# Optimization experiments

Measured on AMD Instinct MI355X. Metric: run time of the kernel, lower is better.

## Reference

```python
import jax, jax.numpy as jnp
import numpy as np

D_MODEL = 1024
N_HEADS = 16
D_HEAD = D_MODEL // N_HEADS
NEG_INF = -1000000000.0


def setup_inputs() -> dict:
    key = jax.random.key(0)
    ks = jax.random.split(key, 12)
    B, S1, S2 = 2, 2048, 2048
    query = jax.random.normal(ks[0], (B, S1, D_MODEL), dtype=jnp.float32)
    k_in = jax.random.normal(ks[1], (B, S2, D_MODEL), dtype=jnp.float32)
    v_in = jax.random.normal(ks[2], (B, S2, D_MODEL), dtype=jnp.float32)
    # causal mask: True = position is masked out (filled with -1e9)
    mask = jnp.broadcast_to(jnp.triu(jnp.ones((S1, S2), dtype=bool), k=1), (B, S1, S2))
    s = 1.0 / np.sqrt(D_MODEL)
    W_q = jax.random.uniform(ks[3], (D_MODEL, D_MODEL), jnp.float32, -s, s)
    b_q = jax.random.uniform(ks[4], (D_MODEL,), jnp.float32, -s, s)
    W_k = jax.random.uniform(ks[5], (D_MODEL, D_MODEL), jnp.float32, -s, s)
    b_k = jax.random.uniform(ks[6], (D_MODEL,), jnp.float32, -s, s)
    W_v = jax.random.uniform(ks[7], (D_MODEL, D_MODEL), jnp.float32, -s, s)
    b_v = jax.random.uniform(ks[8], (D_MODEL,), jnp.float32, -s, s)
    W_o = jax.random.uniform(ks[9], (D_MODEL, D_MODEL), jnp.float32, -s, s)
    b_o = jax.random.uniform(ks[10], (D_MODEL,), jnp.float32, -s, s)
    return {"query": query, "key": k_in, "value": v_in, "mask": mask,
            "W_q": W_q, "b_q": b_q, "W_k": W_k, "b_k": b_k,
            "W_v": W_v, "b_v": b_v, "W_o": W_o, "b_o": b_o}


def reference(query, key, value, mask, W_q, b_q, W_k, b_k, W_v, b_v, W_o, b_o):
    B, S1, _ = query.shape
    S2 = key.shape[1]
    scalar = 1.0 / np.sqrt(D_HEAD)
    # projections (torch Linear: x @ W.T + b)
    Q = (query @ W_q.T + b_q).reshape(B, S1, N_HEADS, D_HEAD).transpose(0, 2, 1, 3)
    K = (key @ W_k.T + b_k).reshape(B, S2, N_HEADS, D_HEAD).transpose(0, 2, 1, 3)
    V = (value @ W_v.T + b_v).reshape(B, S2, N_HEADS, D_HEAD).transpose(0, 2, 1, 3)
    # [B, H, S1, S2]
    scores = jnp.einsum('bhqd,bhkd->bhqk', Q, K) * scalar
    scores = jnp.where(mask[:, None, :, :], NEG_INF, scores)
    probs = jax.nn.softmax(scores, axis=-1)
    attn = jnp.einsum('bhqk,bhkd->bhqd', probs, V)
    concat = attn.transpose(0, 2, 1, 3).reshape(B, S1, D_MODEL)
    return concat @ W_o.T + b_o
```

## Files before the change

### kernel.cpp

```cpp
#include <hip/hip_runtime.h>
#include <hip/hip_bf16.h>
#include <stdint.h>

typedef __bf16 bf16;
typedef __bf16 bf16x8 __attribute__((ext_vector_type(8)));
typedef float f32x4 __attribute__((ext_vector_type(4)));
typedef float f32x16 __attribute__((ext_vector_type(16)));
typedef unsigned int u32;
typedef u32 u32x4 __attribute__((ext_vector_type(4)));

#define D_MODEL 1024
#define S_LEN 2048
#define NB 2
#define NH 16
#define DH 64

__device__ __forceinline__ void gload_lds16(const bf16* g, bf16* l) {
    auto gp = reinterpret_cast<const __attribute__((address_space(1))) unsigned int*>(
        reinterpret_cast<uintptr_t>(g));
    auto lp = reinterpret_cast<__attribute__((address_space(3))) unsigned int*>(
        reinterpret_cast<uintptr_t>(l));
    __builtin_amdgcn_global_load_lds(gp, lp, 16, 0, 0);
}

__device__ __forceinline__ u32 cvtpk(float lo, float hi) {
    u32 r; asm("v_cvt_pk_bf16_f32 %0, %1, %2" : "=v"(r) : "v"(lo), "v"(hi)); return r;
}
__device__ __forceinline__ void plswap(u32& a, u32& b) {
    asm("v_permlane32_swap_b32 %0, %1" : "+v"(a), "+v"(b));
}

__global__ __launch_bounds__(256)
void cvt_all(const float* __restrict__ q, const float* __restrict__ k,
             const float* __restrict__ v, const float* __restrict__ w0,
             const float* __restrict__ w1, const float* __restrict__ w2,
             const float* __restrict__ w3,
             bf16* __restrict__ oq, bf16* __restrict__ ok, bf16* __restrict__ ov,
             bf16* __restrict__ o0, bf16* __restrict__ o1, bf16* __restrict__ o2,
             bf16* __restrict__ o3)
{
    const int bid = blockIdx.x;
    const float* in; bf16* out; int local;
    if (bid < 6144) {
        int r = bid >> 11; local = bid & 2047;
        in  = (r == 0) ? q  : (r == 1) ? k  : v;
        out = (r == 0) ? oq : (r == 1) ? ok : ov;
    } else {
        int wb = bid - 6144;
        int r = wb >> 9; local = wb & 511;
        in  = (r == 0) ? w0 : (r == 1) ? w1 : (r == 2) ? w2 : w3;
        out = (r == 0) ? o0 : (r == 1) ? o1 : (r == 2) ? o2 : o3;
    }
    const size_t i = ((size_t)local * 256 + threadIdx.x) * 8;
    f32x4 x = *(const f32x4*)(in + i);
    f32x4 y = *(const f32x4*)(in + i + 4);
    bf16x8 o;
    #pragma unroll
    for (int j = 0; j < 4; ++j) { o[j] = (bf16)x[j]; o[4 + j] = (bf16)y[j]; }
    *(bf16x8*)(out + i) = o;
}

__global__ __launch_bounds__(256, 2)
void gemm_qkv2(const bf16* __restrict__ Aq, const bf16* __restrict__ Ak, const bf16* __restrict__ Av,
               const bf16* __restrict__ Wq, const bf16* __restrict__ Wk, const bf16* __restrict__ Wv,
               const float* __restrict__ bq, const float* __restrict__ bk, const float* __restrict__ bv,
               bf16* __restrict__ Qo, bf16* __restrict__ KPo, bf16* __restrict__ VPo, float qscale)
{
    __shared__ __align__(16) char gsm[65536];
    bf16* As = (bf16*)gsm;
    bf16* Bs = (bf16*)(gsm + 32768);

    const int K = 1024;
    const int t = threadIdx.x, lane = t & 63, wid = t >> 6;
    const int nbn = 24;
    const int cpx = gridDim.x >> 3;
    const int bid = blockIdx.x;
    const int swz = (bid & 7) * cpx + (bid >> 3);
    const int bm0 = (swz / nbn) << 7;
    const int bn0 = (swz % nbn) << 7;
    const int sel = bn0 >> 10;
    const int nl  = bn0 & 1023;
    const bf16* Ap = (sel == 0) ? Aq : (sel == 1) ? Ak : Av;
    const bf16* Bp = (sel == 0) ? Wq : (sel == 1) ? Wk : Wv;
    const float* bias = (sel == 0) ? bq : (sel == 1) ? bk : bv;

    const int r16 = lane & 15, g = lane >> 4;
    const int wr = (wid >> 1) << 6;
    const int wc = (wid & 1) << 6;

    f32x4 acc[4][4] = {};

    auto stage = [&](int buf, int k0) {
        #pragma unroll
        for (int i = 0; i < 4; ++i) {
            int ch = wid * 256 + i * 64 + lane;
            int row = ch >> 3, c8 = ch & 7;
            int sc = c8 ^ (row & 7);
            gload_lds16(Ap + (size_t)(bm0 + row) * K + k0 + sc * 8, As + buf * 8192 + ch * 8);
            gload_lds16(Bp + (size_t)(nl + row) * K + k0 + sc * 8, Bs + buf * 8192 + ch * 8);
        }
    };

    int cur = 0;
    stage(0, 0);
    for (int k0 = 0; k0 < K; k0 += 64) {
        __syncthreads();
        if (k0 + 64 < K) stage(cur ^ 1, k0 + 64);
        #pragma unroll
        for (int ks = 0; ks < 2; ++ks) {
            const int cl = ks * 4 + g;
            bf16x8 af[4], bfr[4];
            #pragma unroll
            for (int mi = 0; mi < 4; ++mi) {
                int row = wr + mi * 16 + r16;
                af[mi] = *(const bf16x8*)((const char*)As + cur * 16384 + row * 128 + ((cl ^ (row & 7)) << 4));
            }
            #pragma unroll
            for (int ni = 0; ni < 4; ++ni) {
                int row = wc + ni * 16 + r16;
                bfr[ni] = *(const bf16x8*)((const char*)Bs + cur * 16384 + row * 128 + ((cl ^ (row & 7)) << 4));
            }
            #pragma unroll
            for (int mi = 0; mi < 4; ++mi)
                #pragma unroll
                for (int ni = 0; ni < 4; ++ni)
                    acc[mi][ni] = __builtin_amdgcn_mfma_f32_16x16x32_bf16(af[mi], bfr[ni], acc[mi][ni], 0, 0, 0);
        }
        cur ^= 1;
    }

    const int rb = g * 4;
    const int b2 = bm0 >> 11, kt0 = (bm0 & 2047) >> 5;
    if (sel == 0) {
        #pragma unroll
        for (int mi = 0; mi < 4; ++mi) {
            #pragma unroll
            for (int ni = 0; ni < 4; ++ni) {
                int cg = nl + wc + ni * 16 + r16;
                float bv = bias[cg];
                #pragma unroll
                for (int r = 0; r < 4; ++r) {
                    int rg = bm0 + wr + mi * 16 + rb + r;
                    Qo[(size_t)rg * 1024 + cg] = (bf16)((acc[mi][ni][r] + bv) * qscale);
                }
            }
        }
    } else if (sel == 1) {
        __syncthreads();
        bf16* Ts = (bf16*)gsm;
        #pragma unroll
        for (int mi = 0; mi < 4; ++mi)
            #pragma unroll
            for (int ni = 0; ni < 4; ++ni) {
                int dl = wc + ni * 16 + r16;
                float bv = bias[nl + dl];
                #pragma unroll
                for (int r = 0; r < 4; ++r) {
                    int sl = wr + mi * 16 + rb + r;
                    Ts[sl * 136 + dl] = (bf16)(acc[mi][ni][r] + bv);
                }
            }
        __syncthreads();
        #pragma unroll
        for (int i2 = 0; i2 < 8; ++i2) {
            int ch = t + i2 * 256;
            int hloc = ch >> 10, rem = ch & 1023;
            int kt32loc = rem >> 8, db = (rem >> 6) & 3, ln = rem & 63;
            int srcs = kt32loc * 32 + (ln & 31);
            int srcd = hloc * 64 + db * 16 + (ln >> 5) * 8;
            bf16x8 v = *(const bf16x8*)&Ts[srcs * 136 + srcd];
            int bh2 = b2 * 16 + (nl >> 6) + hloc;
            int kt32 = kt0 + kt32loc;
            *(bf16x8*)(KPo + (((size_t)(bh2 * 64 + kt32) * 4 + db) * 64 + ln) * 8) = v;
        }
    } else {
        __syncthreads();
        bf16* Ts = (bf16*)gsm;
        #pragma unroll
        for (int mi = 0; mi < 4; ++mi)
            #pragma unroll
            for (int ni = 0; ni < 4; ++ni) {
                int dl = wc + ni * 16 + r16;
                float bv = bias[nl + dl];
                #pragma unroll
                for (int r = 0; r < 4; ++r) {
                    int sl = wr + mi * 16 + rb + r;
                    Ts[dl * 136 + sl] = (bf16)(acc[mi][ni][r] + bv);
                }
            }
        __syncthreads();
        #pragma unroll
        for (int i2 = 0; i2 < 8; ++i2) {
            int ch = t + i2 * 256;
            int hloc = ch >> 10, rem = ch & 1023;
            int kt32loc = rem >> 8, kb = (rem >> 7) & 1, dt = (rem >> 6) & 1, ln = rem & 63;
            int srcd = hloc * 64 + dt * 32 + (ln & 31);
            int srcs = kt32loc * 32 + kb * 16 + (ln >> 5) * 8;
            bf16x8 v = *(const bf16x8*)&Ts[srcd * 136 + srcs];
            int bh2 = b2 * 16 + (nl >> 6) + hloc;
            int kt32 = kt0 + kt32loc;
            *(bf16x8*)(VPo + ((((size_t)(bh2 * 64 + kt32) * 2 + kb) * 2 + dt) * 64 + ln) * 8) = v;
        }
    }
}

__global__ __launch_bounds__(256)
void gemm_out(const bf16* __restrict__ Ap, const bf16* __restrict__ Bp,
              const float* __restrict__ bias, float* __restrict__ Cp)
{
    __shared__ __align__(16) bf16 As[2][128 * 64];
    __shared__ __align__(16) bf16 Bs[2][64 * 64];

    const int K = 1024, N = 1024;
    const int t = threadIdx.x, lane = t & 63, wid = t >> 6;
    const int nbn = 16;
    const int cpx = gridDim.x >> 3;
    const int bid = blockIdx.x;
    const int swz = (bid & 7) * cpx + (bid >> 3);
    const int bm0 = (swz / nbn) << 7;
    const int bn0 = (swz % nbn) << 6;
    const int r16 = lane & 15, g = lane >> 4;
    const int wr = (wid >> 1) << 6;
    const int wc = (wid & 1) << 5;

    f32x4 acc[4][2] = {};

    auto stage = [&](int buf, int k0) {
        #pragma unroll
        for (int i = 0; i < 4; ++i) {
            int ch = wid * 256 + i * 64 + lane;
            int row = ch >> 3, c8 = ch & 7;
            int sc = c8 ^ (row & 7);
            gload_lds16(Ap + (size_t)(bm0 + row) * K + k0 + sc * 8, &As[buf][ch * 8]);
        }
        #pragma unroll
        for (int i = 0; i < 2; ++i) {
            int ch = wid * 128 + i * 64 + lane;
            int row = ch >> 3, c8 = ch & 7;
            int sc = c8 ^ (row & 7);
            gload_lds16(Bp + (size_t)(bn0 + row) * K + k0 + sc * 8, &Bs[buf][ch * 8]);
        }
    };

    int cur = 0;
    stage(0, 0);
    for (int k0 = 0; k0 < K; k0 += 64) {
        __syncthreads();
        if (k0 + 64 < K) stage(cur ^ 1, k0 + 64);
        #pragma unroll
        for (int ks = 0; ks < 2; ++ks) {
            const int cl = ks * 4 + g;
            bf16x8 af[4], bfr[2];
            #pragma unroll
            for (int mi = 0; mi < 4; ++mi) {
                int row = wr + mi * 16 + r16;
                af[mi] = *(const bf16x8*)((const char*)&As[cur][0] + row * 128 + ((cl ^ (row & 7)) << 4));
            }
            #pragma unroll
            for (int ni = 0; ni < 2; ++ni) {
                int row = wc + ni * 16 + r16;
                bfr[ni] = *(const bf16x8*)((const char*)&Bs[cur][0] + row * 128 + ((cl ^ (row & 7)) << 4));
            }
            #pragma unroll
            for (int mi = 0; mi < 4; ++mi)
                #pragma unroll
                for (int ni = 0; ni < 2; ++ni)
                    acc[mi][ni] = __builtin_amdgcn_mfma_f32_16x16x32_bf16(af[mi], bfr[ni], acc[mi][ni], 0, 0, 0);
        }
        cur ^= 1;
    }

    const int rb = g * 4;
    #pragma unroll
    for (int mi = 0; mi < 4; ++mi) {
        #pragma unroll
        for (int ni = 0; ni < 2; ++ni) {
            int cg = bn0 + wc + ni * 16 + r16;
            float bv = bias[cg];
            #pragma unroll
            for (int r = 0; r < 4; ++r) {
                int rg = bm0 + wr + mi * 16 + rb + r;
                Cp[(size_t)rg * N + cg] = acc[mi][ni][r] + bv;
            }
        }
    }
}

__global__ __launch_bounds__(64, 3)
void attn9(const bf16* __restrict__ Qp, const bf16* __restrict__ KP,
           const bf16* __restrict__ VP, bf16* __restrict__ Pws, float* __restrict__ MLws)
{
    const int lane = threadIdx.x;
    const int l31 = lane & 31, hh = lane >> 5;

    const int bid = blockIdx.x;
    const int xcd = bid & 7, s = bid >> 3;
    const int bh = xcd * 4 + (s & 3);
    const int rest = s >> 2;
    const int jd = rest >> 1, kh = rest & 1;
    const int j = 63 - jd;
    const int b = bh >> 4, h = bh & 15;

    const int nA = (j + 2) >> 1;
    const int r0 = kh ? nA : 0;
    const int r1 = kh ? (j + 1) : nA;

    f32x16 oacc[2] = {};
    float mx = -1e30f, lsum = 0.f;

    if (r0 < r1) {
        bf16x8 qf[4];
        {
            const bf16* qrow = Qp + ((size_t)(b * S_LEN + j * 32 + l31)) * D_MODEL + h * DH + hh * 8;
            #pragma unroll
            for (int db = 0; db < 4; ++db) qf[db] = *(const bf16x8*)(qrow + db * 16);
        }

        const bf16* kp0 = KP + (size_t)bh * 131072 + lane * 8;
        const bf16* vp0 = VP + (size_t)bh * 131072 + lane * 8;

        auto loadK = [&](int tt, bf16x8 (&kf)[4]) {
            const bf16* p = kp0 + (size_t)tt * 2048;
            #pragma unroll
            for (int db = 0; db < 4; ++db) kf[db] = *(const bf16x8*)(p + db * 512);
        };
        auto loadV = [&](int tt, bf16x8 (&vf)[4]) {
            const bf16* p = vp0 + (size_t)tt * 2048;
            #pragma unroll
            for (int q2 = 0; q2 < 4; ++q2) vf[q2] = *(const bf16x8*)(p + q2 * 512);
        };

        auto process = [&](const bf16x8 (&kf)[4], const bf16x8 (&vf)[4], bool diag) {
            f32x16 sacc = {};
            __builtin_amdgcn_s_setprio(1);
            #pragma unroll
            for (int db = 0; db < 4; ++db)
                sacc = __builtin_amdgcn_mfma_f32_32x32x16_bf16(kf[db], qf[db], sacc, 0, 0, 0);
            __builtin_amdgcn_s_setprio(0);
            if (diag) {
                #pragma unroll
                for (int r2 = 0; r2 < 16; ++r2) {
                    int cr = (r2 & 3) + 8 * (r2 >> 2) + 4 * hh;
                    if (cr > l31) sacc[r2] = -1e9f;
                }
            }
            float pm = -3e38f;
            #pragma unroll
            for (int r2 = 0; r2 < 16; ++r2) pm = fmaxf(pm, sacc[r2]);
            pm = fmaxf(pm, __shfl_xor(pm, 32));
            if (__any(pm > mx)) {
                float mnew = fmaxf(mx, pm);
                float al = __builtin_exp2f(mx - mnew);
                lsum *= al;
                #pragma unroll
                for (int dt = 0; dt < 2; ++dt)
                    #pragma unroll
                    for (int r2 = 0; r2 < 16; ++r2) oacc[dt][r2] *= al;
                mx = mnew;
            }
            float ts = 0.f;
            #pragma unroll
            for (int r2 = 0; r2 < 16; ++r2) {
                float p = __builtin_exp2f(sacc[r2] - mx);
                sacc[r2] = p;
                ts += p;
            }
            lsum += ts + __shfl_xor(ts, 32);
            #pragma unroll
            for (int kb = 0; kb < 2; ++kb) {
                u32 w0 = cvtpk(sacc[kb * 8 + 0], sacc[kb * 8 + 1]);
                u32 w2 = cvtpk(sacc[kb * 8 + 4], sacc[kb * 8 + 5]);
                u32 w1 = cvtpk(sacc[kb * 8 + 2], sacc[kb * 8 + 3]);
                u32 w3 = cvtpk(sacc[kb * 8 + 6], sacc[kb * 8 + 7]);
                plswap(w0, w2);
                plswap(w1, w3);
                u32x4 pw; pw[0] = w0; pw[1] = w1; pw[2] = w2; pw[3] = w3;
                bf16x8 pb = __builtin_bit_cast(bf16x8, pw);
                __builtin_amdgcn_s_setprio(1);
                #pragma unroll
                for (int dt = 0; dt < 2; ++dt)
                    oacc[dt] = __builtin_amdgcn_mfma_f32_32x32x16_bf16(vf[kb * 2 + dt], pb, oacc[dt], 0, 0, 0);
                __builtin_amdgcn_s_setprio(0);
            }
        };

        bf16x8 kfA[4], kfB[4], vfA[4], vfB[4];
        loadK(r0, kfA); loadV(r0, vfA);
        int r = r0;
        for (;;) {
            if (r + 1 < r1) { loadK(r + 1, kfB); loadV(r + 1, vfB); }
            process(kfA, vfA, r == j);
            if (++r >= r1) break;
            if (r + 1 < r1) { loadK(r + 1, kfA); loadV(r + 1, vfA); }
            process(kfB, vfB, r == j);
            if (++r >= r1) break;
        }
    }

    const int pid = (bh * 64 + j) * 2 + kh;
    bf16* pb2 = Pws + (size_t)pid * 2048;
    #pragma unroll
    for (int dt = 0; dt < 2; ++dt)
        #pragma unroll
        for (int r2 = 0; r2 < 16; r2 += 2) {
            int d = dt * 32 + (r2 & 3) + 8 * (r2 >> 2) + 4 * hh;
            *(u32*)(pb2 + l31 * 64 + d) = cvtpk(oacc[dt][r2], oacc[dt][r2 + 1]);
        }
    if (hh == 0) {
        MLws[pid * 64 + l31] = mx;
        MLws[pid * 64 + 32 + l31] = lsum;
    }
}

__global__ __launch_bounds__(256)
void attn_merge9(const bf16* __restrict__ Pws, const float* __restrict__ MLws,
                 bf16* __restrict__ Ob)
{
    const int mb = blockIdx.x;
    const int bh = mb >> 6, j = mb & 63;
    const int b = bh >> 4, h = bh & 15;
    const int pidA = (bh * 64 + j) * 2, pidB = pidA + 1;

    const int t = threadIdx.x;
    const int q = t >> 3, c8 = t & 7;
    const float mA = MLws[pidA * 64 + q], lA = MLws[pidA * 64 + 32 + q];
    const float mB = MLws[pidB * 64 + q], lB = MLws[pidB * 64 + 32 + q];
    const float m = fmaxf(mA, mB);
    float a0 = __builtin_exp2f(mA - m), a1 = __builtin_exp2f(mB - m);
    const float linv = 1.0f / (lA * a0 + lB * a1);
    a0 *= linv; a1 *= linv;
    const bf16* pA = Pws + (size_t)pidA * 2048 + q * 64 + c8 * 8;
    const bf16* pB = Pws + (size_t)pidB * 2048 + q * 64 + c8 * 8;
    bf16x8 va = *(const bf16x8*)pA;
    bf16x8 vb = *(const bf16x8*)pB;
    bf16x8 o;
    #pragma unroll
    for (int e = 0; e < 8; ++e)
        o[e] = (bf16)(a0 * (float)va[e] + a1 * (float)vb[e]);
    *(bf16x8*)(Ob + ((size_t)(b * S_LEN + j * 32 + q)) * D_MODEL + h * DH + c8 * 8) = o;
}

extern "C" void kernel_launch(void* const* d_in, const int* in_sizes, int n_in,
                              void* d_out, int out_size, void* d_ws, size_t ws_size,
                              hipStream_t stream)
{
    const float* query = (const float*)d_in[0];
    const float* key   = (const float*)d_in[1];
    const float* value = (const float*)d_in[2];
    const float* W_q = (const float*)d_in[4];
    const float* b_q = (const float*)d_in[5];
    const float* W_k = (const float*)d_in[6];
    const float* b_k = (const float*)d_in[7];
    const float* W_v = (const float*)d_in[8];
    const float* b_v = (const float*)d_in[9];
    const float* W_o = (const float*)d_in[10];
    const float* b_o = (const float*)d_in[11];

    char* w = (char*)d_ws;
    const size_t MB = 1 << 20;
    bf16* qbf = (bf16*)(w);
    bf16* kbf = (bf16*)(w + 8 * MB);
    bf16* vbf = (bf16*)(w + 16 * MB);
    bf16* Qb  = (bf16*)(w + 24 * MB);
    bf16* KP  = (bf16*)(w + 32 * MB);
    bf16* VP  = (bf16*)(w + 40 * MB);
    bf16* Wqb = (bf16*)(w + 48 * MB);
    bf16* Wkb = (bf16*)(w + 50 * MB);
    bf16* Wvb = (bf16*)(w + 52 * MB);
    bf16* Wob = (bf16*)(w + 54 * MB);
    bf16*  Pws  = (bf16*)(w);
    float* MLws = (float*)(w + 16 * MB);
    bf16*  Ob   = (bf16*)(w + 17 * MB);

    dim3 blk(256);
    cvt_all<<<dim3(8192), blk, 0, stream>>>(query, key, value, W_q, W_k, W_v, W_o,
                                            qbf, kbf, vbf, Wqb, Wkb, Wvb, Wob);

    const float qscale = 0.125f * 1.4426950408889634f;
    gemm_qkv2<<<dim3(768), blk, 0, stream>>>(qbf, kbf, vbf, Wqb, Wkb, Wvb,
                                             b_q, b_k, b_v, Qb, KP, VP, qscale);

    attn9<<<dim3(4096), dim3(64), 0, stream>>>(Qb, KP, VP, Pws, MLws);
    attn_merge9<<<dim3(2048), blk, 0, stream>>>(Pws, MLws, Ob);

    gemm_out<<<dim3(512), blk, 0, stream>>>(Ob, Wob, b_o, (float*)d_out);
}
```

Measured before the change: 120.4 us.

## Fuse attention split-K merge into one kernel with 4-wave LDS reduction

Replaces the two-pass attention (single-wave blocks writing partial outputs plus a separate merge kernel) with a 256-thread block where four waves split the key range of a query tile and merge their partial softmax states through shared memory. Each block handles a pair of query tiles (j and 63-j) to balance the causal workload. Q is now written in the same packed per-head layout as K so its fragments load contiguously. This removes the global round trip for partial results and one kernel launch, at the cost of block-level syncs and more shared memory per block.

```diff
diff --git a/kernel.cpp b/kernel.cpp
--- a/kernel.cpp
+++ b/kernel.cpp
@@ -64,7 +64,7 @@
 void gemm_qkv2(const bf16* __restrict__ Aq, const bf16* __restrict__ Ak, const bf16* __restrict__ Av,
                const bf16* __restrict__ Wq, const bf16* __restrict__ Wk, const bf16* __restrict__ Wv,
                const float* __restrict__ bq, const float* __restrict__ bk, const float* __restrict__ bv,
-               bf16* __restrict__ Qo, bf16* __restrict__ KPo, bf16* __restrict__ VPo, float qscale)
+               bf16* __restrict__ QPo, bf16* __restrict__ KPo, bf16* __restrict__ VPo, float qscale)
 {
     __shared__ __align__(16) char gsm[65536];
     bf16* As = (bf16*)gsm;
@@ -131,21 +131,9 @@
 
     const int rb = g * 4;
     const int b2 = bm0 >> 11, kt0 = (bm0 & 2047) >> 5;
-    if (sel == 0) {
-        #pragma unroll
-        for (int mi = 0; mi < 4; ++mi) {
-            #pragma unroll
-            for (int ni = 0; ni < 4; ++ni) {
-                int cg = nl + wc + ni * 16 + r16;
-                float bv = bias[cg];
-                #pragma unroll
-                for (int r = 0; r < 4; ++r) {
-                    int rg = bm0 + wr + mi * 16 + rb + r;
-                    Qo[(size_t)rg * 1024 + cg] = (bf16)((acc[mi][ni][r] + bv) * qscale);
-                }
-            }
-        }
-    } else if (sel == 1) {
+    if (sel != 2) {
+        const float cs = (sel == 0) ? qscale : 1.0f;
+        bf16* dst = (sel == 0) ? QPo : KPo;
         __syncthreads();
         bf16* Ts = (bf16*)gsm;
         #pragma unroll
@@ -157,7 +145,7 @@
                 #pragma unroll
                 for (int r = 0; r < 4; ++r) {
                     int sl = wr + mi * 16 + rb + r;
-                    Ts[sl * 136 + dl] = (bf16)(acc[mi][ni][r] + bv);
+                    Ts[sl * 136 + dl] = (bf16)((acc[mi][ni][r] + bv) * cs);
                 }
             }
         __syncthreads();
@@ -171,7 +159,7 @@
             bf16x8 v = *(const bf16x8*)&Ts[srcs * 136 + srcd];
             int bh2 = b2 * 16 + (nl >> 6) + hloc;
             int kt32 = kt0 + kt32loc;
-            *(bf16x8*)(KPo + (((size_t)(bh2 * 64 + kt32) * 4 + db) * 64 + ln) * 8) = v;
+            *(bf16x8*)(dst + (((size_t)(bh2 * 64 + kt32) * 4 + db) * 64 + ln) * 8) = v;
         }
     } else {
         __syncthreads();
@@ -286,158 +274,150 @@
     }
 }
 
-__global__ __launch_bounds__(64, 3)
-void attn9(const bf16* __restrict__ Qp, const bf16* __restrict__ KP,
-           const bf16* __restrict__ VP, bf16* __restrict__ Pws, float* __restrict__ MLws)
+__global__ __launch_bounds__(256, 4)
+void attn10(const bf16* __restrict__ QP, const bf16* __restrict__ KP,
+            const bf16* __restrict__ VP, bf16* __restrict__ Ob)
 {
-    const int lane = threadIdx.x;
+    __shared__ float Of[4][64][33];
+    __shared__ float mlS[4][2][32];
+
+    const int t = threadIdx.x, lane = t & 63, wv = t >> 6;
     const int l31 = lane & 31, hh = lane >> 5;
 
     const int bid = blockIdx.x;
     const int xcd = bid & 7, s = bid >> 3;
     const int bh = xcd * 4 + (s & 3);
-    const int rest = s >> 2;
-    const int jd = rest >> 1, kh = rest & 1;
-    const int j = 63 - jd;
+    const int jp = s >> 2;
     const int b = bh >> 4, h = bh & 15;
 
-    const int nA = (j + 2) >> 1;
-    const int r0 = kh ? nA : 0;
-    const int r1 = kh ? (j + 1) : nA;
-
-    f32x16 oacc[2] = {};
-    float mx = -1e30f, lsum = 0.f;
-
-    if (r0 < r1) {
-        bf16x8 qf[4];
+    const bf16* kp0 = KP + (size_t)bh * 131072 + lane * 8;
+    const bf16* vp0 = VP + (size_t)bh * 131072 + lane * 8;
+
+    #pragma unroll 1
+    for (int ph = 0; ph < 2; ++ph) {
+        const int J = ph ? (63 - jp) : jp;
+        const int n = J + 1;
+        const int r0 = (wv * n) >> 2;
+        const int r1 = ((wv + 1) * n) >> 2;
+
+        f32x16 oacc[2] = {};
+        float mx = -1e30f, lsum = 0.f;
+
+        if (r0 < r1) {
+            bf16x8 qf[4];
+            {
+                const bf16* qp = QP + ((size_t)(bh * 64 + J) * 4) * 512 + lane * 8;
+                #pragma unroll
+                for (int db = 0; db < 4; ++db) qf[db] = *(const bf16x8*)(qp + db * 512);
+            }
+
+            auto loadK = [&](int tt, bf16x8 (&kf)[4]) {
+                const bf16* p = kp0 + (size_t)tt * 2048;
+                #pragma unroll
+                for (int db = 0; db < 4; ++db) kf[db] = *(const bf16x8*)(p + db * 512);
+            };
+            auto loadV = [&](int tt, bf16x8 (&vf)[4]) {
+                const bf16* p = vp0 + (size_t)tt * 2048;
+                #pragma unroll
+                for (int q2 = 0; q2 < 4; ++q2) vf[q2] = *(const bf16x8*)(p + q2 * 512);
+            };
+
+            auto process = [&](const bf16x8 (&kf)[4], const bf16x8 (&vf)[4], bool diag) {
+                f32x16 sacc = {};
+                __builtin_amdgcn_s_setprio(1);
+                #pragma unroll
+                for (int db = 0; db < 4; ++db)
+                    sacc = __builtin_amdgcn_mfma_f32_32x32x16_bf16(kf[db], qf[db], sacc, 0, 0, 0);
+                __builtin_amdgcn_s_setprio(0);
+                if (diag) {
+                    #pragma unroll
+                    for (int r2 = 0; r2 < 16; ++r2) {
+                        int cr = (r2 & 3) + 8 * (r2 >> 2) + 4 * hh;
+                        if (cr > l31) sacc[r2] = -1e9f;
+                    }
+                }
+                float pm = -3e38f;
+                #pragma unroll
+                for (int r2 = 0; r2 < 16; ++r2) pm = fmaxf(pm, sacc[r2]);
+                pm = fmaxf(pm, __shfl_xor(pm, 32));
+                if (__any(pm > mx)) {
+                    float mnew = fmaxf(mx, pm);
+                    float al = __builtin_exp2f(mx - mnew);
+                    lsum *= al;
+                    #pragma unroll
+                    for (int dt = 0; dt < 2; ++dt)
+                        #pragma unroll
+                        for (int r2 = 0; r2 < 16; ++r2) oacc[dt][r2] *= al;
+                    mx = mnew;
+                }
+                float ts = 0.f;
+                #pragma unroll
+                for (int r2 = 0; r2 < 16; ++r2) {
+                    float p = __builtin_exp2f(sacc[r2] - mx);
+                    sacc[r2] = p;
+                    ts += p;
+                }
+                lsum += ts + __shfl_xor(ts, 32);
+                #pragma unroll
+                for (int kb = 0; kb < 2; ++kb) {
+                    u32 w0 = cvtpk(sacc[kb * 8 + 0], sacc[kb * 8 + 1]);
+                    u32 w2 = cvtpk(sacc[kb * 8 + 4], sacc[kb * 8 + 5]);
+                    u32 w1 = cvtpk(sacc[kb * 8 + 2], sacc[kb * 8 + 3]);
+                    u32 w3 = cvtpk(sacc[kb * 8 + 6], sacc[kb * 8 + 7]);
+                    plswap(w0, w2);
+                    plswap(w1, w3);
+                    u32x4 pw; pw[0] = w0; pw[1] = w1; pw[2] = w2; pw[3] = w3;
+                    bf16x8 pb = __builtin_bit_cast(bf16x8, pw);
+                    __builtin_amdgcn_s_setprio(1);
+                    #pragma unroll
+                    for (int dt = 0; dt < 2; ++dt)
+                        oacc[dt] = __builtin_amdgcn_mfma_f32_32x32x16_bf16(vf[kb * 2 + dt], pb, oacc[dt], 0, 0, 0);
+                    __builtin_amdgcn_s_setprio(0);
+                }
+            };
+
+            bf16x8 kfA[4], kfB[4], vfA[4], vfB[4];
+            loadK(r0, kfA); loadV(r0, vfA);
+            int r = r0;
+            for (;;) {
+                if (r + 1 < r1) { loadK(r + 1, kfB); loadV(r + 1, vfB); }
+                process(kfA, vfA, r == J);
+                if (++r >= r1) break;
+                if (r + 1 < r1) { loadK(r + 1, kfA); loadV(r + 1, vfA); }
+                process(kfB, vfB, r == J);
+                if (++r >= r1) break;
+            }
+        }
+
+        #pragma unroll
+        for (int dt = 0; dt < 2; ++dt)
+            #pragma unroll
+            for (int r2 = 0; r2 < 16; ++r2) {
+                int d = dt * 32 + (r2 & 3) + 8 * (r2 >> 2) + 4 * hh;
+                Of[wv][d][l31] = oacc[dt][r2];
+            }
+        if (hh == 0) { mlS[wv][0][l31] = mx; mlS[wv][1][l31] = lsum; }
+        __syncthreads();
+
         {
-            const bf16* qrow = Qp + ((size_t)(b * S_LEN + j * 32 + l31)) * D_MODEL + h * DH + hh * 8;
-            #pragma unroll
-            for (int db = 0; db < 4; ++db) qf[db] = *(const bf16x8*)(qrow + db * 16);
-        }
-
-        const bf16* kp0 = KP + (size_t)bh * 131072 + lane * 8;
-        const bf16* vp0 = VP + (size_t)bh * 131072 + lane * 8;
-
-        auto loadK = [&](int tt, bf16x8 (&kf)[4]) {
-            const bf16* p = kp0 + (size_t)tt * 2048;
-            #pragma unroll
-            for (int db = 0; db < 4; ++db) kf[db] = *(const bf16x8*)(p + db * 512);
-        };
-        auto loadV = [&](int tt, bf16x8 (&vf)[4]) {
-            const bf16* p = vp0 + (size_t)tt * 2048;
-            #pragma unroll
-            for (int q2 = 0; q2 < 4; ++q2) vf[q2] = *(const bf16x8*)(p + q2 * 512);
-        };
-
-        auto process = [&](const bf16x8 (&kf)[4], const bf16x8 (&vf)[4], bool diag) {
-            f32x16 sacc = {};
-            __builtin_amdgcn_s_setprio(1);
-            #pragma unroll
-            for (int db = 0; db < 4; ++db)
-                sacc = __builtin_amdgcn_mfma_f32_32x32x16_bf16(kf[db], qf[db], sacc, 0, 0, 0);
-            __builtin_amdgcn_s_setprio(0);
-            if (diag) {
-                #pragma unroll
-                for (int r2 = 0; r2 < 16; ++r2) {
-                    int cr = (r2 & 3) + 8 * (r2 >> 2) + 4 * hh;
-                    if (cr > l31) sacc[r2] = -1e9f;
-                }
-            }
-            float pm = -3e38f;
-            #pragma unroll
-            for (int r2 = 0; r2 < 16; ++r2) pm = fmaxf(pm, sacc[r2]);
-            pm = fmaxf(pm, __shfl_xor(pm, 32));
-            if (__any(pm > mx)) {
-                float mnew = fmaxf(mx, pm);
-                float al = __builtin_exp2f(mx - mnew);
-                lsum *= al;
-                #pragma unroll
-                for (int dt = 0; dt < 2; ++dt)
-                    #pragma unroll
-                    for (int r2 = 0; r2 < 16; ++r2) oacc[dt][r2] *= al;
-                mx = mnew;
-            }
-            float ts = 0.f;
-            #pragma unroll
-            for (int r2 = 0; r2 < 16; ++r2) {
-                float p = __builtin_exp2f(sacc[r2] - mx);
-                sacc[r2] = p;
-                ts += p;
-            }
-            lsum += ts + __shfl_xor(ts, 32);
-            #pragma unroll
-            for (int kb = 0; kb < 2; ++kb) {
-                u32 w0 = cvtpk(sacc[kb * 8 + 0], sacc[kb * 8 + 1]);
-                u32 w2 = cvtpk(sacc[kb * 8 + 4], sacc[kb * 8 + 5]);
-                u32 w1 = cvtpk(sacc[kb * 8 + 2], sacc[kb * 8 + 3]);
-                u32 w3 = cvtpk(sacc[kb * 8 + 6], sacc[kb * 8 + 7]);
-                plswap(w0, w2);
-                plswap(w1, w3);
-                u32x4 pw; pw[0] = w0; pw[1] = w1; pw[2] = w2; pw[3] = w3;
-                bf16x8 pb = __builtin_bit_cast(bf16x8, pw);
-                __builtin_amdgcn_s_setprio(1);
-                #pragma unroll
-                for (int dt = 0; dt < 2; ++dt)
-                    oacc[dt] = __builtin_amdgcn_mfma_f32_32x32x16_bf16(vf[kb * 2 + dt], pb, oacc[dt], 0, 0, 0);
-                __builtin_amdgcn_s_setprio(0);
-            }
-        };
-
-        bf16x8 kfA[4], kfB[4], vfA[4], vfB[4];
-        loadK(r0, kfA); loadV(r0, vfA);
-        int r = r0;
-        for (;;) {
-            if (r + 1 < r1) { loadK(r + 1, kfB); loadV(r + 1, vfB); }
-            process(kfA, vfA, r == j);
-            if (++r >= r1) break;
-            if (r + 1 < r1) { loadK(r + 1, kfA); loadV(r + 1, vfA); }
-            process(kfB, vfB, r == j);
-            if (++r >= r1) break;
-        }
-    }
-
-    const int pid = (bh * 64 + j) * 2 + kh;
-    bf16* pb2 = Pws + (size_t)pid * 2048;
-    #pragma unroll
-    for (int dt = 0; dt < 2; ++dt)
-        #pragma unroll
-        for (int r2 = 0; r2 < 16; r2 += 2) {
-            int d = dt * 32 + (r2 & 3) + 8 * (r2 >> 2) + 4 * hh;
-            *(u32*)(pb2 + l31 * 64 + d) = cvtpk(oacc[dt][r2], oacc[dt][r2 + 1]);
-        }
-    if (hh == 0) {
-        MLws[pid * 64 + l31] = mx;
-        MLws[pid * 64 + 32 + l31] = lsum;
-    }
-}
-
-__global__ __launch_bounds__(256)
-void attn_merge9(const bf16* __restrict__ Pws, const float* __restrict__ MLws,
-                 bf16* __restrict__ Ob)
-{
-    const int mb = blockIdx.x;
-    const int bh = mb >> 6, j = mb & 63;
-    const int b = bh >> 4, h = bh & 15;
-    const int pidA = (bh * 64 + j) * 2, pidB = pidA + 1;
-
-    const int t = threadIdx.x;
-    const int q = t >> 3, c8 = t & 7;
-    const float mA = MLws[pidA * 64 + q], lA = MLws[pidA * 64 + 32 + q];
-    const float mB = MLws[pidB * 64 + q], lB = MLws[pidB * 64 + 32 + q];
-    const float m = fmaxf(mA, mB);
-    float a0 = __builtin_exp2f(mA - m), a1 = __builtin_exp2f(mB - m);
-    const float linv = 1.0f / (lA * a0 + lB * a1);
-    a0 *= linv; a1 *= linv;
-    const bf16* pA = Pws + (size_t)pidA * 2048 + q * 64 + c8 * 8;
-    const bf16* pB = Pws + (size_t)pidB * 2048 + q * 64 + c8 * 8;
-    bf16x8 va = *(const bf16x8*)pA;
-    bf16x8 vb = *(const bf16x8*)pB;
-    bf16x8 o;
-    #pragma unroll
-    for (int e = 0; e < 8; ++e)
-        o[e] = (bf16)(a0 * (float)va[e] + a1 * (float)vb[e]);
-    *(bf16x8*)(Ob + ((size_t)(b * S_LEN + j * 32 + q)) * D_MODEL + h * DH + c8 * 8) = o;
+            const int q = t >> 3, c8 = t & 7;
+            float mA = mlS[0][0][q], mB = mlS[1][0][q], mC = mlS[2][0][q], mD = mlS[3][0][q];
+            float m = fmaxf(fmaxf(mA, mB), fmaxf(mC, mD));
+            float a0 = __builtin_exp2f(mA - m), a1 = __builtin_exp2f(mB - m);
+            float a2 = __builtin_exp2f(mC - m), a3 = __builtin_exp2f(mD - m);
+            float l = mlS[0][1][q] * a0 + mlS[1][1][q] * a1 + mlS[2][1][q] * a2 + mlS[3][1][q] * a3;
+            float inv = 1.0f / l;
+            bf16x8 o8;
+            #pragma unroll
+            for (int i = 0; i < 8; ++i) {
+                int d = c8 * 8 + i;
+                float o = a0 * Of[0][d][q] + a1 * Of[1][d][q] + a2 * Of[2][d][q] + a3 * Of[3][d][q];
+                o8[i] = (bf16)(o * inv);
+            }
+            *(bf16x8*)(Ob + ((size_t)(b * S_LEN + J * 32 + q)) * D_MODEL + h * DH + c8 * 8) = o8;
+        }
+        __syncthreads();
+    }
 }
 
 extern "C" void kernel_launch(void* const* d_in, const int* in_sizes, int n_in,
@@ -461,16 +441,14 @@
     bf16* qbf = (bf16*)(w);
     bf16* kbf = (bf16*)(w + 8 * MB);
     bf16* vbf = (bf16*)(w + 16 * MB);
-    bf16* Qb  = (bf16*)(w + 24 * MB);
+    bf16* QP  = (bf16*)(w + 24 * MB);
     bf16* KP  = (bf16*)(w + 32 * MB);
     bf16* VP  = (bf16*)(w + 40 * MB);
     bf16* Wqb = (bf16*)(w + 48 * MB);
     bf16* Wkb = (bf16*)(w + 50 * MB);
     bf16* Wvb = (bf16*)(w + 52 * MB);
     bf16* Wob = (bf16*)(w + 54 * MB);
-    bf16*  Pws  = (bf16*)(w);
-    float* MLws = (float*)(w + 16 * MB);
-    bf16*  Ob   = (bf16*)(w + 17 * MB);
+    bf16* Ob  = (bf16*)(w);
 
     dim3 blk(256);
     cvt_all<<<dim3(8192), blk, 0, stream>>>(query, key, value, W_q, W_k, W_v, W_o,
@@ -478,10 +456,9 @@
 
     const float qscale = 0.125f * 1.4426950408889634f;
     gemm_qkv2<<<dim3(768), blk, 0, stream>>>(qbf, kbf, vbf, Wqb, Wkb, Wvb,
-                                             b_q, b_k, b_v, Qb, KP, VP, qscale);
-
-    attn9<<<dim3(4096), dim3(64), 0, stream>>>(Qb, KP, VP, Pws, MLws);
-    attn_merge9<<<dim3(2048), blk, 0, stream>>>(Pws, MLws, Ob);
+                                             b_q, b_k, b_v, QP, KP, VP, qscale);
+
+    attn10<<<dim3(1024), blk, 0, stream>>>(QP, KP, VP, Ob);
 
     gemm_out<<<dim3(512), blk, 0, stream>>>(Ob, Wob, b_o, (float*)d_out);
 }
```

Result: slower. 242.0 us (+101.0%).
